# Performance work log

Measured on AMD Instinct MI355X. Metric: run time of the kernel, lower is better.

## Reference

```python
import jax, jax.numpy as jnp
import numpy as np

DIM = 512
DIM_INNER = 512
NUM_HEADS = 16
HEAD_DIM = DIM_INNER // NUM_HEADS  # 32


def setup_inputs() -> dict:
    key = jax.random.key(0)
    k1, k2, k3, k4 = jax.random.split(key, 4)
    b, n = 1, 4096
    x = jax.random.normal(k1, (b, n, DIM), dtype=jnp.float32)
    # torch nn.Linear weights, stored as (in, out) so y = x @ W (+ b)
    s_qkv = 1.0 / np.sqrt(DIM)
    W_qkv = jax.random.uniform(k2, (DIM, DIM_INNER * 3), jnp.float32, -s_qkv, s_qkv)
    W_a = jax.random.uniform(k3, (DIM, NUM_HEADS * 2), jnp.float32, -s_qkv, s_qkv)
    b_a = jax.random.uniform(k4, (NUM_HEADS * 2,), jnp.float32, -s_qkv, s_qkv)
    return {"x": x, "W_qkv": W_qkv, "W_a": W_a, "b_a": b_a}


def _gate_loop(q, k, v, a):
    # q,k,v: (bh, n, d) float32; a: (bh, n, 1, 1) complex64
    kv = jnp.einsum('bnd,bne->bnde', k, v).astype(jnp.complex64)  # (bh, n, d, d)

    def binop(ei, ej):
        a_i, kv_i = ei
        a_j, kv_j = ej
        return a_j * a_i, a_j * kv_i + kv_j

    _, kv = jax.lax.associative_scan(binop, (a, kv), axis=1)
    return jnp.einsum('bnd,bnde->bne', q, kv.real)


def reference(x, W_qkv, W_a, b_a):
    b, n, _ = x.shape
    h, d = NUM_HEADS, HEAD_DIM

    qkv = x @ W_qkv                                   # (b, n, 3*dim_inner)
    q, k, v = jnp.split(qkv, 3, axis=-1)

    def to_heads(t):  # 'b n (h d) -> (b h) n d'
        return t.reshape(b, n, h, d).transpose(0, 2, 1, 3).reshape(b * h, n, d)

    q, k, v = map(to_heads, (q, k, v))

    a_lin = x @ W_a + b_a                             # (b, n, 2h)
    a_ri = a_lin.reshape(b, n, h, 2)
    a_c = jax.lax.complex(a_ri[..., 0], a_ri[..., 1])  # (b, n, h)
    mag = jnp.abs(a_c)
    ph = jnp.angle(a_c)
    gate = jax.lax.complex(jnp.cos(ph), jnp.sin(ph)) * jax.nn.sigmoid(mag).astype(jnp.complex64)
    gate = gate.transpose(0, 2, 1).reshape(b * h, n, 1, 1)  # '(b h) n 1 1'

    out = _gate_loop(q, k, v, gate)                   # (bh, n, d)
    out = out.reshape(b, h, n, d).transpose(0, 2, 1, 3).reshape(b, n, h * d)
    # out_proj is Identity since dim_inner == dim
    return out
```

## Files before the change

kernel.cpp:

```cpp
#include <hip/hip_runtime.h>
#include <hip/hip_bf16.h>

#define SEQ    4096
#define DIM    512
#define DIM3   1536
#define NH     16
#define HD     32
#define CHUNK  64
#define NCHUNK (SEQ / CHUNK)

typedef __attribute__((ext_vector_type(8))) short short8;
typedef __attribute__((ext_vector_type(4))) float f32x4;
typedef __attribute__((ext_vector_type(4))) unsigned short u16x4;
typedef __attribute__((ext_vector_type(4))) unsigned int u32x4;

__device__ inline unsigned short f2bf(float f) {
  unsigned u = __builtin_bit_cast(unsigned, f);
  unsigned r = (u + 0x7fff + ((u >> 16) & 1)) >> 16;
  return (unsigned short)r;
}
__device__ inline float bf2f(unsigned short b) {
  unsigned u = ((unsigned)b) << 16;
  return __builtin_bit_cast(float, u);
}

__global__ __launch_bounds__(256) void gl_cvt_gate(
    const float* __restrict__ x, const float* __restrict__ W,
    const float* __restrict__ Wa, const float* __restrict__ ba,
    unsigned short* __restrict__ xb, unsigned short* __restrict__ Wt,
    float2* __restrict__ graw) {
  __shared__ union {
    float wtile[32][33];
    struct { float xs[4][DIM]; float red[4][8][32]; } g;
  } sm;
  int b = blockIdx.x;
  if (b < 1024) {
    const int n0 = b * 4;
    const int tid = threadIdx.x;
    const float4* xv = (const float4*)(x + (size_t)n0 * DIM);
    u16x4* xbo = (u16x4*)(xb + (size_t)n0 * DIM);
    float4* xsv = (float4*)&sm.g.xs[0][0];
    for (int i = tid; i < 512; i += 256) {
      float4 v = xv[i];
      xsv[i] = v;
      u16x4 o = {f2bf(v.x), f2bf(v.y), f2bf(v.z), f2bf(v.w)};
      xbo[i] = o;
    }
    __syncthreads();
    const int o = tid & 31, s = tid >> 5;
    float pr[4] = {0, 0, 0, 0};
    for (int k = s * 64; k < s * 64 + 64; ++k) {
      float w = Wa[k * 32 + o];
      #pragma unroll
      for (int r = 0; r < 4; ++r) pr[r] += sm.g.xs[r][k] * w;
    }
    #pragma unroll
    for (int r = 0; r < 4; ++r) sm.g.red[r][s][o] = pr[r];
    __syncthreads();
    if (tid < 128) {
      int r = tid >> 5, oo = tid & 31;
      float acc = ba[oo];
      #pragma unroll
      for (int ss = 0; ss < 8; ++ss) acc += sm.g.red[r][ss][oo];
      sm.g.red[r][0][oo] = acc;
    }
    __syncthreads();
    if (tid < 64) {
      int r = tid >> 4, hh = tid & 15;
      float re = sm.g.red[r][0][2 * hh], im = sm.g.red[r][0][2 * hh + 1];
      float mag = sqrtf(re * re + im * im);
      float lml = -log1pf(expf(-mag));
      float ph = atan2f(im, re);
      graw[(size_t)hh * SEQ + n0 + r] = make_float2(lml, ph);
    }
  } else {
    b -= 1024;
    int bx = b % 48, by = b / 48;
    int tx = threadIdx.x & 31, ty = threadIdx.x >> 5;
    for (int i = ty; i < 32; i += 8)
      sm.wtile[i][tx] = W[(size_t)(by * 32 + i) * DIM3 + bx * 32 + tx];
    __syncthreads();
    for (int i = ty; i < 32; i += 8)
      Wt[(size_t)(bx * 32 + i) * DIM + by * 32 + tx] = f2bf(sm.wtile[tx][i]);
  }
}

#define GBM 64
#define GBN 128
#define GBK 64
__global__ __launch_bounds__(256) void gl_gemm_mfma(
    const unsigned short* __restrict__ A, const unsigned short* __restrict__ Bt,
    unsigned short* __restrict__ C) {
  __shared__ unsigned short As[2][GBM * GBK];
  __shared__ unsigned short Bs[2][GBN * GBK];
  const int tid = threadIdx.x;
  const int id = blockIdx.x;
  const int tile = (id & 7) * 96 + (id >> 3);
  const int by = tile / 12, bx = tile % 12;
  const int row0 = by * GBM, col0 = bx * GBN;
  const int wid = tid >> 6, lane = tid & 63;
  const int wr = wid >> 1, wc = wid & 1;
  const int lr = lane & 15, lg = lane >> 4;

  auto stage = [&](int buf, int t) {
    const int k0 = t * GBK;
    #pragma unroll
    for (int i = 0; i < 2; ++i) {
      int byteoff = i * 4096 + tid * 16;
      int row = byteoff >> 7;
      int logslot = ((byteoff >> 4) & 7) ^ (row & 7);
      const unsigned short* gp = A + (size_t)(row0 + row) * DIM + k0 + logslot * 8;
      __builtin_amdgcn_global_load_lds(
          (const __attribute__((address_space(1))) void*)gp,
          (__attribute__((address_space(3))) void*)((char*)As[buf] + byteoff),
          16, 0, 0);
    }
    #pragma unroll
    for (int i = 0; i < 4; ++i) {
      int byteoff = i * 4096 + tid * 16;
      int row = byteoff >> 7;
      int logslot = ((byteoff >> 4) & 7) ^ (row & 7);
      const unsigned short* gp = Bt + (size_t)(col0 + row) * DIM + k0 + logslot * 8;
      __builtin_amdgcn_global_load_lds(
          (const __attribute__((address_space(1))) void*)gp,
          (__attribute__((address_space(3))) void*)((char*)Bs[buf] + byteoff),
          16, 0, 0);
    }
  };

  f32x4 acc[2][4] = {};
  stage(0, 0);

  #pragma unroll
  for (int t = 0; t < 8; ++t) {
    const int p = t & 1;
    if (t < 7) {
      stage(p ^ 1, t + 1);
      asm volatile("s_waitcnt vmcnt(6)" ::: "memory");
    } else {
      asm volatile("s_waitcnt vmcnt(0)" ::: "memory");
    }
    __syncthreads();
    const char* AsB = (const char*)As[p];
    const char* BsB = (const char*)Bs[p];
    #pragma unroll
    for (int ks = 0; ks < 2; ++ks) {
      short8 af[2], bfr[4];
      #pragma unroll
      for (int m = 0; m < 2; ++m) {
        int row = wr * 32 + m * 16 + lr;
        int ps = (ks * 4 + lg) ^ (row & 7);
        af[m] = *(const short8*)(AsB + row * 128 + ps * 16);
      }
      #pragma unroll
      for (int n = 0; n < 4; ++n) {
        int col = wc * 64 + n * 16 + lr;
        int ps = (ks * 4 + lg) ^ (col & 7);
        bfr[n] = *(const short8*)(BsB + col * 128 + ps * 16);
      }
      #pragma unroll
      for (int m = 0; m < 2; ++m)
        #pragma unroll
        for (int n = 0; n < 4; ++n)
          acc[m][n] = __builtin_amdgcn_mfma_f32_16x16x32_bf16(
              af[m], bfr[n], acc[m][n], 0, 0, 0);
    }
    __syncthreads();
  }

  #pragma unroll
  for (int m = 0; m < 2; ++m)
    #pragma unroll
    for (int n = 0; n < 4; ++n) {
      int grow0 = row0 + wr * 32 + m * 16 + lg * 4;
      int gcol = col0 + wc * 64 + n * 16 + lr;
      #pragma unroll
      for (int j = 0; j < 4; ++j)
        C[(size_t)(grow0 + j) * DIM3 + gcol] = f2bf(acc[m][n][j]);
    }
}

__global__ __launch_bounds__(128) void gl_pass1(
    const unsigned short* __restrict__ qkv, const float2* __restrict__ graw,
    float2* __restrict__ LmPh, float* __restrict__ SLre,
    float* __restrict__ SLim, float2* __restrict__ Aprod) {
  const int b = blockIdx.x;
  const int c = b & (NCHUNK - 1), h = b >> 6;
  const int tid = threadIdx.x, w = tid >> 6, lane = tid & 63;
  const int lr = lane & 15, lg = lane >> 4;
  const int n0 = c * CHUNK;
  __shared__ float2 lmph[CHUNK];

  float2 g = graw[(size_t)h * SEQ + n0 + lane];
  float lm = g.x, ph = g.y;
  #pragma unroll
  for (int off = 1; off < 64; off <<= 1) {
    float a = __shfl_up(lm, off), p = __shfl_up(ph, off);
    if (lane >= off) { lm += a; ph += p; }
  }
  if (w == 0) {
    LmPh[(size_t)h * SEQ + n0 + lane] = make_float2(lm, ph);
    lmph[lane] = make_float2(lm, ph);
    if (lane == 63) {
      float e = __expf(lm);
      Aprod[h * NCHUNK + c] = make_float2(e * __cosf(ph), e * __sinf(ph));
    }
  }
  __syncthreads();
  const float2 end = lmph[63];

  const size_t rowb = (size_t)n0 * DIM3 + h * HD;
  f32x4 acc[2][2] = {};
  #pragma unroll
  for (int ks = 0; ks < 2; ++ks) {
    const int jb = ks * 32 + lg * 8;
    float wv[8];
    #pragma unroll
    for (int jj = 0; jj < 8; ++jj) {
      float2 lp = lmph[jb + jj];
      float e = __expf(end.x - lp.x);
      float an = end.y - lp.y;
      wv[jj] = e * (w == 0 ? __cosf(an) : __sinf(an));
    }
    short8 afr[2], bfr[2];
    #pragma unroll
    for (int mt = 0; mt < 2; ++mt) {
      int d = mt * 16 + lr;
      unsigned u0, u1, u2, u3;
      #define LD_KW(q) ((unsigned)f2bf(bf2f(qkv[rowb + (size_t)(jb + 2*(q)) * DIM3 + DIM + d]) * wv[2*(q)]) | \
                        ((unsigned)f2bf(bf2f(qkv[rowb + (size_t)(jb + 2*(q)+1) * DIM3 + DIM + d]) * wv[2*(q)+1]) << 16))
      u0 = LD_KW(0); u1 = LD_KW(1); u2 = LD_KW(2); u3 = LD_KW(3);
      #undef LD_KW
      u32x4 t = {u0, u1, u2, u3};
      afr[mt] = __builtin_bit_cast(short8, t);
    }
    #pragma unroll
    for (int nt = 0; nt < 2; ++nt) {
      int e_ = nt * 16 + lr;
      unsigned u0, u1, u2, u3;
      #define LD_V(q) ((unsigned)qkv[rowb + (size_t)(jb + 2*(q)) * DIM3 + 2*DIM + e_] | \
                       ((unsigned)qkv[rowb + (size_t)(jb + 2*(q)+1) * DIM3 + 2*DIM + e_] << 16))
      u0 = LD_V(0); u1 = LD_V(1); u2 = LD_V(2); u3 = LD_V(3);
      #undef LD_V
      u32x4 t = {u0, u1, u2, u3};
      bfr[nt] = __builtin_bit_cast(short8, t);
    }
    #pragma unroll
    for (int mt = 0; mt < 2; ++mt)
      #pragma unroll
      for (int nt = 0; nt < 2; ++nt)
        acc[mt][nt] = __builtin_amdgcn_mfma_f32_16x16x32_bf16(
            afr[mt], bfr[nt], acc[mt][nt], 0, 0, 0);
  }
  float* dst = (w == 0) ? SLre : SLim;
  const size_t base = (size_t)(h * NCHUNK + c) * (HD * HD);
  #pragma unroll
  for (int mt = 0; mt < 2; ++mt)
    #pragma unroll
    for (int nt = 0; nt < 2; ++nt)
      #pragma unroll
      for (int r = 0; r < 4; ++r) {
        int d = mt * 16 + lg * 4 + r, e_ = nt * 16 + lr;
        dst[base + d * HD + e_] = acc[mt][nt][r];
      }
}

__global__ __launch_bounds__(128) void gl_scan_chunks(
    const float* __restrict__ SLre, const float* __restrict__ SLim,
    const float2* __restrict__ Aprod, unsigned* __restrict__ SinPre,
    unsigned* __restrict__ SinPim) {
  const int h = blockIdx.x >> 3;
  const int oct = blockIdx.x & 7;
  const int tid = threadIdx.x;
  const int elem = oct * 128 + tid;
  const int e = elem & 31;
  const int qp = elem >> 6;
  const bool lo = !(tid & 32);
  const size_t hb = (size_t)h * NCHUNK * (HD * HD) + elem;
  const float2* AP = Aprod + h * NCHUNK;
  float2 s = make_float2(0.f, 0.f);
  for (int cg = 0; cg < NCHUNK; cg += 8) {
    float lre[8], lim[8];
    float2 a[8];
    #pragma unroll
    for (int j = 0; j < 8; ++j) {
      size_t off = hb + (size_t)(cg + j) * (HD * HD);
      lre[j] = SLre[off];
      lim[j] = SLim[off];
      a[j] = AP[cg + j];
    }
    #pragma unroll
    for (int j = 0; j < 8; ++j) {
      float px = __shfl_xor(s.x, 32);
      float py = __shfl_xor(s.y, 32);
      if (lo) {
        size_t wo = (size_t)(h * NCHUNK + cg + j) * 512 + qp * 32 + e;
        SinPre[wo] = (unsigned)f2bf(s.x) | ((unsigned)f2bf(px) << 16);
        SinPim[wo] = (unsigned)f2bf(s.y) | ((unsigned)f2bf(py) << 16);
      }
      float re = s.x, im = s.y;
      s.x = a[j].x * re - a[j].y * im + lre[j];
      s.y = a[j].x * im + a[j].y * re + lim[j];
    }
  }
}

__global__ __launch_bounds__(128) void gl_pass2(
    const unsigned short* __restrict__ qkv, const float2* __restrict__ LmPh,
    const unsigned* __restrict__ SinPre, const unsigned* __restrict__ SinPim,
    float* __restrict__ out) {
  const int b = blockIdx.x;
  const int c = b & (NCHUNK - 1), h = b >> 6;
  const int tid = threadIdx.x, w = tid >> 6, lane = tid & 63;
  const int lr = lane & 15, lg = lane >> 4;
  const int n0 = c * CHUNK;
  __shared__ float2 lmph[CHUNK];
  __shared__ unsigned Pp[32][68];
  if (tid < 64) lmph[tid] = LmPh[(size_t)h * SEQ + n0 + tid];
  __syncthreads();

  const size_t rowb = (size_t)n0 * DIM3 + h * HD;
  short8 kf[2], qf[4];
  #pragma unroll
  for (int mt = 0; mt < 2; ++mt) {
    int j = (2 * w + mt) * 16 + lr;
    kf[mt] = *(const short8*)(qkv + rowb + (size_t)j * DIM3 + DIM + lg * 8);
  }
  #pragma unroll
  for (int nt = 0; nt < 4; ++nt) {
    int n = nt * 16 + lr;
    qf[nt] = *(const short8*)(qkv + rowb + (size_t)n * DIM3 + lg * 8);
  }
  f32x4 pacc[2][4] = {};
  #pragma unroll
  for (int mt = 0; mt < 2; ++mt)
    #pragma unroll
    for (int nt = 0; nt < 4; ++nt)
      pacc[mt][nt] = __builtin_amdgcn_mfma_f32_16x16x32_bf16(
          kf[mt], qf[nt], pacc[mt][nt], 0, 0, 0);

  #pragma unroll
  for (int mt = 0; mt < 2; ++mt) {
    int jt = 2 * w + mt;
    #pragma unroll
    for (int r2 = 0; r2 < 2; ++r2) {
      int j0 = jt * 16 + lg * 4 + 2 * r2;
      float2 lj0 = lmph[j0], lj1 = lmph[j0 + 1];
      #pragma unroll
      for (int nt = 0; nt < 4; ++nt) {
        int n = nt * 16 + lr;
        float2 ln = lmph[n];
        float w0 = (j0 <= n) ? __expf(ln.x - lj0.x) * __cosf(ln.y - lj0.y) : 0.f;
        float w1 = (j0 + 1 <= n) ? __expf(ln.x - lj1.x) * __cosf(ln.y - lj1.y) : 0.f;
        Pp[jt * 8 + lg * 2 + r2][n] =
            (unsigned)f2bf(pacc[mt][nt][2 * r2] * w0) |
            ((unsigned)f2bf(pacc[mt][nt][2 * r2 + 1] * w1) << 16);
      }
    }
  }
  __syncthreads();

  const size_t s512 = (size_t)(h * NCHUNK + c) * 512;
  short8 sre[2], sim[2];
  #pragma unroll
  for (int nt = 0; nt < 2; ++nt) {
    int e_ = nt * 16 + lr;
    unsigned ur[4], ui[4];
    #pragma unroll
    for (int q = 0; q < 4; ++q) {
      ur[q] = SinPre[s512 + (size_t)(lg * 4 + q) * 32 + e_];
      ui[q] = SinPim[s512 + (size_t)(lg * 4 + q) * 32 + e_];
    }
    u32x4 tr = {ur[0], ur[1], ur[2], ur[3]};
    u32x4 ti = {ui[0], ui[1], ui[2], ui[3]};
    sre[nt] = __builtin_bit_cast(short8, tr);
    sim[nt] = __builtin_bit_cast(short8, ti);
  }
  f32x4 ore[2][2] = {}, oim[2][2] = {};
  #pragma unroll
  for (int mt = 0; mt < 2; ++mt)
    #pragma unroll
    for (int nt = 0; nt < 2; ++nt) {
      ore[mt][nt] = __builtin_amdgcn_mfma_f32_16x16x32_bf16(
          qf[2 * w + mt], sre[nt], ore[mt][nt], 0, 0, 0);
      oim[mt][nt] = __builtin_amdgcn_mfma_f32_16x16x32_bf16(
          qf[2 * w + mt], sim[nt], oim[mt][nt], 0, 0, 0);
    }
  f32x4 oacc[2][2];
  #pragma unroll
  for (int mt = 0; mt < 2; ++mt)
    #pragma unroll
    for (int r = 0; r < 4; ++r) {
      int n = (2 * w + mt) * 16 + lg * 4 + r;
      float2 ln = lmph[n];
      float eg = __expf(ln.x);
      float gr = eg * __cosf(ln.y), gi = eg * __sinf(ln.y);
      oacc[mt][0][r] = gr * ore[mt][0][r] - gi * oim[mt][0][r];
      oacc[mt][1][r] = gr * ore[mt][1][r] - gi * oim[mt][1][r];
    }
  #pragma unroll
  for (int ks = 0; ks < 2; ++ks) {
    short8 pa[2];
    #pragma unroll
    for (int mt = 0; mt < 2; ++mt) {
      int n_ = (2 * w + mt) * 16 + lr;
      unsigned u0 = Pp[ks * 16 + lg * 4 + 0][n_];
      unsigned u1 = Pp[ks * 16 + lg * 4 + 1][n_];
      unsigned u2 = Pp[ks * 16 + lg * 4 + 2][n_];
      unsigned u3 = Pp[ks * 16 + lg * 4 + 3][n_];
      u32x4 t = {u0, u1, u2, u3};
      pa[mt] = __builtin_bit_cast(short8, t);
    }
    const int jb = ks * 32 + lg * 8;
    short8 vf[2];
    #pragma unroll
    for (int nt = 0; nt < 2; ++nt) {
      int e_ = nt * 16 + lr;
      unsigned u0, u1, u2, u3;
      #define LD_V(q) ((unsigned)qkv[rowb + (size_t)(jb + 2*(q)) * DIM3 + 2*DIM + e_] | \
                       ((unsigned)qkv[rowb + (size_t)(jb + 2*(q)+1) * DIM3 + 2*DIM + e_] << 16))
      u0 = LD_V(0); u1 = LD_V(1); u2 = LD_V(2); u3 = LD_V(3);
      #undef LD_V
      u32x4 t = {u0, u1, u2, u3};
      vf[nt] = __builtin_bit_cast(short8, t);
    }
    #pragma unroll
    for (int mt = 0; mt < 2; ++mt)
      #pragma unroll
      for (int nt = 0; nt < 2; ++nt)
        oacc[mt][nt] = __builtin_amdgcn_mfma_f32_16x16x32_bf16(
            pa[mt], vf[nt], oacc[mt][nt], 0, 0, 0);
  }
  #pragma unroll
  for (int mt = 0; mt < 2; ++mt)
    #pragma unroll
    for (int nt = 0; nt < 2; ++nt)
      #pragma unroll
      for (int r = 0; r < 4; ++r) {
        int n = (2 * w + mt) * 16 + lg * 4 + r;
        int e_ = nt * 16 + lr;
        out[(size_t)(n0 + n) * DIM + h * HD + e_] = oacc[mt][nt][r];
      }
}

extern "C" void kernel_launch(void* const* d_in, const int* in_sizes, int n_in,
                              void* d_out, int out_size, void* d_ws,
                              size_t ws_size, hipStream_t stream) {
  const float* x     = (const float*)d_in[0];
  const float* W_qkv = (const float*)d_in[1];
  const float* W_a   = (const float*)d_in[2];
  const float* b_a   = (const float*)d_in[3];
  float* out = (float*)d_out;

  char* ws = (char*)d_ws;
  unsigned short* qkv  = (unsigned short*)ws;
  float2* graw  = (float2*)(ws + 12582912);
  float2* LmPh  = (float2*)(ws + 13107200);
  float*  SLre  = (float*)(ws + 13631488);
  float*  SLim  = (float*)(ws + 17825792);
  float2* Aprod = (float2*)(ws + 22020096);
  unsigned* SinPre = (unsigned*)(ws + 22028288);
  unsigned* SinPim = (unsigned*)(ws + 24125440);
  unsigned short* xb = (unsigned short*)(ws + 26222592);
  unsigned short* Wt = (unsigned short*)(ws + 30416896);

  gl_cvt_gate<<<1792, 256, 0, stream>>>(x, W_qkv, W_a, b_a, xb, Wt, graw);
  gl_gemm_mfma<<<768, 256, 0, stream>>>(xb, Wt, qkv);
  gl_pass1<<<NCHUNK * NH, 128, 0, stream>>>(qkv, graw, LmPh, SLre, SLim, Aprod);
  gl_scan_chunks<<<128, 128, 0, stream>>>(SLre, SLim, Aprod, SinPre, SinPim);
  gl_pass2<<<NCHUNK * NH, 128, 0, stream>>>(qkv, LmPh, SinPre, SinPim, out);
}
```

Measured before the change: 52.84 us.

## Fuse chunk passes into cooperative kernel with grid syncs; enlarge GEMM tile

Replaces the three chunked-scan kernels (pass1, chunk scan, pass2) with one cooperative kernel. Each block handles two chunks of a head, keeps K/V and the gate prefix sums in shared memory across phases, and separates the phases with grid-wide syncs. This removes two kernel launches and the reload of K/V and gate data between passes. The QKV GEMM tile also grows from 64x128 to 128x128, halving the block count and giving each wave more MFMA work. The risks are the cost of grid.sync, only 128 of 512 blocks working during the scan phase, and higher register pressure in the GEMM.

```diff
diff --git a/kernel.cpp b/kernel.cpp
--- a/kernel.cpp
+++ b/kernel.cpp
@@ -1,5 +1,8 @@
 #include <hip/hip_runtime.h>
 #include <hip/hip_bf16.h>
+#include <hip/hip_cooperative_groups.h>
+
+namespace cg = cooperative_groups;
 
 #define SEQ    4096
 #define DIM    512
@@ -85,17 +88,17 @@
   }
 }
 
-#define GBM 64
+#define GBM 128
 #define GBN 128
 #define GBK 64
 __global__ __launch_bounds__(256) void gl_gemm_mfma(
     const unsigned short* __restrict__ A, const unsigned short* __restrict__ Bt,
     unsigned short* __restrict__ C) {
   __shared__ unsigned short As[2][GBM * GBK];
-  __shared__ unsigned short Bs[2][GBN * GBK];
+  __shared__ unsigned short Bs[2][GBM * GBK];
   const int tid = threadIdx.x;
   const int id = blockIdx.x;
-  const int tile = (id & 7) * 96 + (id >> 3);
+  const int tile = (id & 7) * 48 + (id >> 3);
   const int by = tile / 12, bx = tile % 12;
   const int row0 = by * GBM, col0 = bx * GBN;
   const int wid = tid >> 6, lane = tid & 63;
@@ -105,7 +108,7 @@
   auto stage = [&](int buf, int t) {
     const int k0 = t * GBK;
     #pragma unroll
-    for (int i = 0; i < 2; ++i) {
+    for (int i = 0; i < 4; ++i) {
       int byteoff = i * 4096 + tid * 16;
       int row = byteoff >> 7;
       int logslot = ((byteoff >> 4) & 7) ^ (row & 7);
@@ -128,7 +131,7 @@
     }
   };
 
-  f32x4 acc[2][4] = {};
+  f32x4 acc[4][4] = {};
   stage(0, 0);
 
   #pragma unroll
@@ -136,7 +139,7 @@
     const int p = t & 1;
     if (t < 7) {
       stage(p ^ 1, t + 1);
-      asm volatile("s_waitcnt vmcnt(6)" ::: "memory");
+      asm volatile("s_waitcnt vmcnt(8)" ::: "memory");
     } else {
       asm volatile("s_waitcnt vmcnt(0)" ::: "memory");
     }
@@ -145,10 +148,10 @@
     const char* BsB = (const char*)Bs[p];
     #pragma unroll
     for (int ks = 0; ks < 2; ++ks) {
-      short8 af[2], bfr[4];
-      #pragma unroll
-      for (int m = 0; m < 2; ++m) {
-        int row = wr * 32 + m * 16 + lr;
+      short8 af[4], bfr[4];
+      #pragma unroll
+      for (int m = 0; m < 4; ++m) {
+        int row = wr * 64 + m * 16 + lr;
         int ps = (ks * 4 + lg) ^ (row & 7);
         af[m] = *(const short8*)(AsB + row * 128 + ps * 16);
       }
@@ -159,7 +162,7 @@
         bfr[n] = *(const short8*)(BsB + col * 128 + ps * 16);
       }
       #pragma unroll
-      for (int m = 0; m < 2; ++m)
+      for (int m = 0; m < 4; ++m)
         #pragma unroll
         for (int n = 0; n < 4; ++n)
           acc[m][n] = __builtin_amdgcn_mfma_f32_16x16x32_bf16(
@@ -169,15 +172,287 @@
   }
 
   #pragma unroll
-  for (int m = 0; m < 2; ++m)
+  for (int m = 0; m < 4; ++m)
     #pragma unroll
     for (int n = 0; n < 4; ++n) {
-      int grow0 = row0 + wr * 32 + m * 16 + lg * 4;
+      int grow0 = row0 + wr * 64 + m * 16 + lg * 4;
       int gcol = col0 + wc * 64 + n * 16 + lr;
       #pragma unroll
       for (int j = 0; j < 4; ++j)
         C[(size_t)(grow0 + j) * DIM3 + gcol] = f2bf(acc[m][n][j]);
     }
+}
+
+__global__ __launch_bounds__(128) void gl_fused(
+    const unsigned short* __restrict__ qkv, const float2* __restrict__ graw,
+    float* __restrict__ SLre, float* __restrict__ SLim,
+    float2* __restrict__ Aprod, unsigned* __restrict__ SinPre,
+    unsigned* __restrict__ SinPim, float* __restrict__ out) {
+  cg::grid_group grid = cg::this_grid();
+  const int b = blockIdx.x;
+  const int tid = threadIdx.x, w = tid >> 6, lane = tid & 63;
+  const int lr = lane & 15, lg = lane >> 4;
+  const int h = b >> 5;
+  const int c0 = (b & 31) * 2;
+
+  __shared__ unsigned short Ksm[2][CHUNK][HD];
+  __shared__ unsigned short Vsm[2][CHUNK][HD];
+  __shared__ float2 lmph[2][CHUNK];
+  __shared__ unsigned Pp[32][68];
+
+  {
+    const int c = c0 + w;
+    float2 g = graw[(size_t)h * SEQ + c * CHUNK + lane];
+    float lm = g.x, ph = g.y;
+    #pragma unroll
+    for (int off = 1; off < 64; off <<= 1) {
+      float a = __shfl_up(lm, off), p = __shfl_up(ph, off);
+      if (lane >= off) { lm += a; ph += p; }
+    }
+    lmph[w][lane] = make_float2(lm, ph);
+    if (lane == 63) {
+      float e = __expf(lm);
+      Aprod[h * NCHUNK + c] = make_float2(e * __cosf(ph), e * __sinf(ph));
+    }
+  }
+
+  #pragma unroll
+  for (int cc = 0; cc < 2; ++cc) {
+    const size_t rb = (size_t)(c0 + cc) * CHUNK * DIM3 + h * HD;
+    for (int i = tid; i < CHUNK * HD / 4; i += 128) {
+      int row = i >> 3, e4 = (i & 7) * 4;
+      *(u16x4*)&Ksm[cc][row][e4] =
+          *(const u16x4*)(qkv + rb + (size_t)row * DIM3 + DIM + e4);
+      *(u16x4*)&Vsm[cc][row][e4] =
+          *(const u16x4*)(qkv + rb + (size_t)row * DIM3 + 2 * DIM + e4);
+    }
+  }
+  __syncthreads();
+
+  #pragma unroll
+  for (int cc = 0; cc < 2; ++cc) {
+    const float2 end = lmph[cc][63];
+    f32x4 acc[2][2] = {};
+    #pragma unroll
+    for (int ks = 0; ks < 2; ++ks) {
+      const int jb = ks * 32 + lg * 8;
+      float wv[8];
+      #pragma unroll
+      for (int jj = 0; jj < 8; ++jj) {
+        float2 lp = lmph[cc][jb + jj];
+        float e = __expf(end.x - lp.x);
+        float an = end.y - lp.y;
+        wv[jj] = e * (w == 0 ? __cosf(an) : __sinf(an));
+      }
+      short8 afr[2], bfr[2];
+      #pragma unroll
+      for (int mt = 0; mt < 2; ++mt) {
+        int d = mt * 16 + lr;
+        unsigned uu[4];
+        #pragma unroll
+        for (int q = 0; q < 4; ++q)
+          uu[q] = (unsigned)f2bf(bf2f(Ksm[cc][jb + 2 * q][d]) * wv[2 * q]) |
+                  ((unsigned)f2bf(bf2f(Ksm[cc][jb + 2 * q + 1][d]) * wv[2 * q + 1]) << 16);
+        u32x4 t = {uu[0], uu[1], uu[2], uu[3]};
+        afr[mt] = __builtin_bit_cast(short8, t);
+      }
+      #pragma unroll
+      for (int nt = 0; nt < 2; ++nt) {
+        int e_ = nt * 16 + lr;
+        unsigned uu[4];
+        #pragma unroll
+        for (int q = 0; q < 4; ++q)
+          uu[q] = (unsigned)Vsm[cc][jb + 2 * q][e_] |
+                  ((unsigned)Vsm[cc][jb + 2 * q + 1][e_] << 16);
+        u32x4 t = {uu[0], uu[1], uu[2], uu[3]};
+        bfr[nt] = __builtin_bit_cast(short8, t);
+      }
+      #pragma unroll
+      for (int mt = 0; mt < 2; ++mt)
+        #pragma unroll
+        for (int nt = 0; nt < 2; ++nt)
+          acc[mt][nt] = __builtin_amdgcn_mfma_f32_16x16x32_bf16(
+              afr[mt], bfr[nt], acc[mt][nt], 0, 0, 0);
+    }
+    float* dst = (w == 0) ? SLre : SLim;
+    const size_t base = (size_t)(h * NCHUNK + c0 + cc) * (HD * HD);
+    #pragma unroll
+    for (int mt = 0; mt < 2; ++mt)
+      #pragma unroll
+      for (int nt = 0; nt < 2; ++nt)
+        #pragma unroll
+        for (int r = 0; r < 4; ++r) {
+          int d = mt * 16 + lg * 4 + r, e_ = nt * 16 + lr;
+          dst[base + d * HD + e_] = acc[mt][nt][r];
+        }
+  }
+  grid.sync();
+
+  if (b < 128) {
+    const int sh = b >> 3;
+    const int oct = b & 7;
+    const int elem = oct * 128 + tid;
+    const int e = elem & 31;
+    const int qp = elem >> 6;
+    const bool lo = !(tid & 32);
+    const size_t hb = (size_t)sh * NCHUNK * (HD * HD) + elem;
+    const float2* AP = Aprod + sh * NCHUNK;
+    float2 s = make_float2(0.f, 0.f);
+    for (int cgp = 0; cgp < NCHUNK; cgp += 8) {
+      float lre[8], lim[8];
+      float2 a[8];
+      #pragma unroll
+      for (int j = 0; j < 8; ++j) {
+        size_t off = hb + (size_t)(cgp + j) * (HD * HD);
+        lre[j] = SLre[off];
+        lim[j] = SLim[off];
+        a[j] = AP[cgp + j];
+      }
+      #pragma unroll
+      for (int j = 0; j < 8; ++j) {
+        float px = __shfl_xor(s.x, 32);
+        float py = __shfl_xor(s.y, 32);
+        if (lo) {
+          size_t wo = (size_t)(sh * NCHUNK + cgp + j) * 512 + qp * 32 + e;
+          SinPre[wo] = (unsigned)f2bf(s.x) | ((unsigned)f2bf(px) << 16);
+          SinPim[wo] = (unsigned)f2bf(s.y) | ((unsigned)f2bf(py) << 16);
+        }
+        float re = s.x, im = s.y;
+        s.x = a[j].x * re - a[j].y * im + lre[j];
+        s.y = a[j].x * im + a[j].y * re + lim[j];
+      }
+    }
+  }
+  grid.sync();
+
+  #pragma unroll
+  for (int cc = 0; cc < 2; ++cc) {
+    const int c = c0 + cc;
+    const int n0 = c * CHUNK;
+    const size_t rowb = (size_t)n0 * DIM3 + h * HD;
+    short8 kf[2], qf[4];
+    #pragma unroll
+    for (int mt = 0; mt < 2; ++mt) {
+      int j = (2 * w + mt) * 16 + lr;
+      kf[mt] = *(const short8*)&Ksm[cc][j][lg * 8];
+    }
+    #pragma unroll
+    for (int nt = 0; nt < 4; ++nt) {
+      int n = nt * 16 + lr;
+      qf[nt] = *(const short8*)(qkv + rowb + (size_t)n * DIM3 + lg * 8);
+    }
+    f32x4 pacc[2][4] = {};
+    #pragma unroll
+    for (int mt = 0; mt < 2; ++mt)
+      #pragma unroll
+      for (int nt = 0; nt < 4; ++nt)
+        pacc[mt][nt] = __builtin_amdgcn_mfma_f32_16x16x32_bf16(
+            kf[mt], qf[nt], pacc[mt][nt], 0, 0, 0);
+
+    __syncthreads();
+    #pragma unroll
+    for (int mt = 0; mt < 2; ++mt) {
+      int jt = 2 * w + mt;
+      #pragma unroll
+      for (int r2 = 0; r2 < 2; ++r2) {
+        int j0 = jt * 16 + lg * 4 + 2 * r2;
+        float2 lj0 = lmph[cc][j0], lj1 = lmph[cc][j0 + 1];
+        #pragma unroll
+        for (int nt = 0; nt < 4; ++nt) {
+          int n = nt * 16 + lr;
+          float2 ln = lmph[cc][n];
+          float w0 = (j0 <= n) ? __expf(ln.x - lj0.x) * __cosf(ln.y - lj0.y) : 0.f;
+          float w1 = (j0 + 1 <= n) ? __expf(ln.x - lj1.x) * __cosf(ln.y - lj1.y) : 0.f;
+          Pp[jt * 8 + lg * 2 + r2][n] =
+              (unsigned)f2bf(pacc[mt][nt][2 * r2] * w0) |
+              ((unsigned)f2bf(pacc[mt][nt][2 * r2 + 1] * w1) << 16);
+        }
+      }
+    }
+    __syncthreads();
+
+    const size_t s512 = (size_t)(h * NCHUNK + c) * 512;
+    short8 sre[2], sim[2];
+    #pragma unroll
+    for (int nt = 0; nt < 2; ++nt) {
+      int e_ = nt * 16 + lr;
+      unsigned ur[4], ui[4];
+      #pragma unroll
+      for (int q = 0; q < 4; ++q) {
+        ur[q] = SinPre[s512 + (size_t)(lg * 4 + q) * 32 + e_];
+        ui[q] = SinPim[s512 + (size_t)(lg * 4 + q) * 32 + e_];
+      }
+      u32x4 tr = {ur[0], ur[1], ur[2], ur[3]};
+      u32x4 ti = {ui[0], ui[1], ui[2], ui[3]};
+      sre[nt] = __builtin_bit_cast(short8, tr);
+      sim[nt] = __builtin_bit_cast(short8, ti);
+    }
+    f32x4 ore[2][2] = {}, oim[2][2] = {};
+    #pragma unroll
+    for (int mt = 0; mt < 2; ++mt)
+      #pragma unroll
+      for (int nt = 0; nt < 2; ++nt) {
+        ore[mt][nt] = __builtin_amdgcn_mfma_f32_16x16x32_bf16(
+            qf[2 * w + mt], sre[nt], ore[mt][nt], 0, 0, 0);
+        oim[mt][nt] = __builtin_amdgcn_mfma_f32_16x16x32_bf16(
+            qf[2 * w + mt], sim[nt], oim[mt][nt], 0, 0, 0);
+      }
+    f32x4 oacc[2][2];
+    #pragma unroll
+    for (int mt = 0; mt < 2; ++mt)
+      #pragma unroll
+      for (int r = 0; r < 4; ++r) {
+        int n = (2 * w + mt) * 16 + lg * 4 + r;
+        float2 ln = lmph[cc][n];
+        float eg = __expf(ln.x);
+        float gr = eg * __cosf(ln.y), gi = eg * __sinf(ln.y);
+        oacc[mt][0][r] = gr * ore[mt][0][r] - gi * oim[mt][0][r];
+        oacc[mt][1][r] = gr * ore[mt][1][r] - gi * oim[mt][1][r];
+      }
+    #pragma unroll
+    for (int ks = 0; ks < 2; ++ks) {
+      short8 pa[2];
+      #pragma unroll
+      for (int mt = 0; mt < 2; ++mt) {
+        int n_ = (2 * w + mt) * 16 + lr;
+        unsigned u0 = Pp[ks * 16 + lg * 4 + 0][n_];
+        unsigned u1 = Pp[ks * 16 + lg * 4 + 1][n_];
+        unsigned u2 = Pp[ks * 16 + lg * 4 + 2][n_];
+        unsigned u3 = Pp[ks * 16 + lg * 4 + 3][n_];
+        u32x4 t = {u0, u1, u2, u3};
+        pa[mt] = __builtin_bit_cast(short8, t);
+      }
+      const int jb = ks * 32 + lg * 8;
+      short8 vf[2];
+      #pragma unroll
+      for (int nt = 0; nt < 2; ++nt) {
+        int e_ = nt * 16 + lr;
+        unsigned uu[4];
+        #pragma unroll
+        for (int q = 0; q < 4; ++q)
+          uu[q] = (unsigned)Vsm[cc][jb + 2 * q][e_] |
+                  ((unsigned)Vsm[cc][jb + 2 * q + 1][e_] << 16);
+        u32x4 t = {uu[0], uu[1], uu[2], uu[3]};
+        vf[nt] = __builtin_bit_cast(short8, t);
+      }
+      #pragma unroll
+      for (int mt = 0; mt < 2; ++mt)
+        #pragma unroll
+        for (int nt = 0; nt < 2; ++nt)
+          oacc[mt][nt] = __builtin_amdgcn_mfma_f32_16x16x32_bf16(
+              pa[mt], vf[nt], oacc[mt][nt], 0, 0, 0);
+    }
+    #pragma unroll
+    for (int mt = 0; mt < 2; ++mt)
+      #pragma unroll
+      for (int nt = 0; nt < 2; ++nt)
+        #pragma unroll
+        for (int r = 0; r < 4; ++r) {
+          int n = (2 * w + mt) * 16 + lg * 4 + r;
+          int e_ = nt * 16 + lr;
+          out[(size_t)(n0 + n) * DIM + h * HD + e_] = oacc[mt][nt][r];
+        }
+  }
 }
 
 __global__ __launch_bounds__(128) void gl_pass1(
@@ -465,8 +740,15 @@
   unsigned short* Wt = (unsigned short*)(ws + 30416896);
 
   gl_cvt_gate<<<1792, 256, 0, stream>>>(x, W_qkv, W_a, b_a, xb, Wt, graw);
-  gl_gemm_mfma<<<768, 256, 0, stream>>>(xb, Wt, qkv);
-  gl_pass1<<<NCHUNK * NH, 128, 0, stream>>>(qkv, graw, LmPh, SLre, SLim, Aprod);
-  gl_scan_chunks<<<128, 128, 0, stream>>>(SLre, SLim, Aprod, SinPre, SinPim);
-  gl_pass2<<<NCHUNK * NH, 128, 0, stream>>>(qkv, LmPh, SinPre, SinPim, out);
-}
+  gl_gemm_mfma<<<384, 256, 0, stream>>>(xb, Wt, qkv);
+
+  void* kargs[] = {(void*)&qkv, (void*)&graw, (void*)&SLre, (void*)&SLim,
+                   (void*)&Aprod, (void*)&SinPre, (void*)&SinPim, (void*)&out};
+  hipError_t err = hipLaunchCooperativeKernel((void*)gl_fused, dim3(512),
+                                              dim3(128), kargs, 0, stream);
+  if (err != hipSuccess) {
+    gl_pass1<<<NCHUNK * NH, 128, 0, stream>>>(qkv, graw, LmPh, SLre, SLim, Aprod);
+    gl_scan_chunks<<<128, 128, 0, stream>>>(SLre, SLim, Aprod, SinPre, SinPim);
+    gl_pass2<<<NCHUNK * NH, 128, 0, stream>>>(qkv, LmPh, SinPre, SinPim, out);
+  }
+}
```

New measurement: 180.1 us. 3.41x slower.

## Enlarge GEMM M-tile to 128 and stage K/V chunks in LDS for scan passes

Applied to the files above, without the earlier changes.

The QKV GEMM tile grows from 64x128 to 128x128, halving the grid to 384 blocks and doubling per-wave accumulators so operand data is reused more. In pass1 and pass2, K and V chunk slices are now loaded cooperatively into shared memory with vectorized loads, replacing the scattered per-element global 16-bit gathers. The prefix scan in pass1 now runs only in wave 0. The goal is fewer global transactions and better GEMM data reuse, at the cost of fewer GEMM blocks (384 on a 256-CU part, which may leave the second wave partly idle) and more LDS per block.

```diff
diff --git a/kernel.cpp b/kernel.cpp
--- a/kernel.cpp
+++ b/kernel.cpp
@@ -85,17 +85,17 @@
   }
 }
 
-#define GBM 64
+#define GBM 128
 #define GBN 128
 #define GBK 64
 __global__ __launch_bounds__(256) void gl_gemm_mfma(
     const unsigned short* __restrict__ A, const unsigned short* __restrict__ Bt,
     unsigned short* __restrict__ C) {
   __shared__ unsigned short As[2][GBM * GBK];
-  __shared__ unsigned short Bs[2][GBN * GBK];
+  __shared__ unsigned short Bs[2][GBM * GBK];
   const int tid = threadIdx.x;
   const int id = blockIdx.x;
-  const int tile = (id & 7) * 96 + (id >> 3);
+  const int tile = (id & 7) * 48 + (id >> 3);
   const int by = tile / 12, bx = tile % 12;
   const int row0 = by * GBM, col0 = bx * GBN;
   const int wid = tid >> 6, lane = tid & 63;
@@ -105,7 +105,7 @@
   auto stage = [&](int buf, int t) {
     const int k0 = t * GBK;
     #pragma unroll
-    for (int i = 0; i < 2; ++i) {
+    for (int i = 0; i < 4; ++i) {
       int byteoff = i * 4096 + tid * 16;
       int row = byteoff >> 7;
       int logslot = ((byteoff >> 4) & 7) ^ (row & 7);
@@ -128,7 +128,7 @@
     }
   };
 
-  f32x4 acc[2][4] = {};
+  f32x4 acc[4][4] = {};
   stage(0, 0);
 
   #pragma unroll
@@ -136,7 +136,7 @@
     const int p = t & 1;
     if (t < 7) {
       stage(p ^ 1, t + 1);
-      asm volatile("s_waitcnt vmcnt(6)" ::: "memory");
+      asm volatile("s_waitcnt vmcnt(8)" ::: "memory");
     } else {
       asm volatile("s_waitcnt vmcnt(0)" ::: "memory");
     }
@@ -145,10 +145,10 @@
     const char* BsB = (const char*)Bs[p];
     #pragma unroll
     for (int ks = 0; ks < 2; ++ks) {
-      short8 af[2], bfr[4];
-      #pragma unroll
-      for (int m = 0; m < 2; ++m) {
-        int row = wr * 32 + m * 16 + lr;
+      short8 af[4], bfr[4];
+      #pragma unroll
+      for (int m = 0; m < 4; ++m) {
+        int row = wr * 64 + m * 16 + lr;
         int ps = (ks * 4 + lg) ^ (row & 7);
         af[m] = *(const short8*)(AsB + row * 128 + ps * 16);
       }
@@ -159,7 +159,7 @@
         bfr[n] = *(const short8*)(BsB + col * 128 + ps * 16);
       }
       #pragma unroll
-      for (int m = 0; m < 2; ++m)
+      for (int m = 0; m < 4; ++m)
         #pragma unroll
         for (int n = 0; n < 4; ++n)
           acc[m][n] = __builtin_amdgcn_mfma_f32_16x16x32_bf16(
@@ -169,10 +169,10 @@
   }
 
   #pragma unroll
-  for (int m = 0; m < 2; ++m)
+  for (int m = 0; m < 4; ++m)
     #pragma unroll
     for (int n = 0; n < 4; ++n) {
-      int grow0 = row0 + wr * 32 + m * 16 + lg * 4;
+      int grow0 = row0 + wr * 64 + m * 16 + lg * 4;
       int gcol = col0 + wc * 64 + n * 16 + lr;
       #pragma unroll
       for (int j = 0; j < 4; ++j)
@@ -190,17 +190,28 @@
   const int lr = lane & 15, lg = lane >> 4;
   const int n0 = c * CHUNK;
   __shared__ float2 lmph[CHUNK];
-
-  float2 g = graw[(size_t)h * SEQ + n0 + lane];
-  float lm = g.x, ph = g.y;
-  #pragma unroll
-  for (int off = 1; off < 64; off <<= 1) {
-    float a = __shfl_up(lm, off), p = __shfl_up(ph, off);
-    if (lane >= off) { lm += a; ph += p; }
-  }
+  __shared__ unsigned short Ksm[CHUNK][34];
+  __shared__ unsigned short Vsm[CHUNK][34];
+
+  const size_t rb = (size_t)n0 * DIM3 + h * HD;
+  for (int i = tid; i < 512; i += 128) {
+    int row = i >> 3, e4 = (i & 7) * 4;
+    *(u16x4*)&Ksm[row][e4] =
+        *(const u16x4*)(qkv + rb + (size_t)row * DIM3 + DIM + e4);
+    *(u16x4*)&Vsm[row][e4] =
+        *(const u16x4*)(qkv + rb + (size_t)row * DIM3 + 2 * DIM + e4);
+  }
+
   if (w == 0) {
+    float2 g = graw[(size_t)h * SEQ + n0 + lane];
+    float lm = g.x, ph = g.y;
+    #pragma unroll
+    for (int off = 1; off < 64; off <<= 1) {
+      float a = __shfl_up(lm, off), p = __shfl_up(ph, off);
+      if (lane >= off) { lm += a; ph += p; }
+    }
+    lmph[lane] = make_float2(lm, ph);
     LmPh[(size_t)h * SEQ + n0 + lane] = make_float2(lm, ph);
-    lmph[lane] = make_float2(lm, ph);
     if (lane == 63) {
       float e = __expf(lm);
       Aprod[h * NCHUNK + c] = make_float2(e * __cosf(ph), e * __sinf(ph));
@@ -209,7 +220,6 @@
   __syncthreads();
   const float2 end = lmph[63];
 
-  const size_t rowb = (size_t)n0 * DIM3 + h * HD;
   f32x4 acc[2][2] = {};
   #pragma unroll
   for (int ks = 0; ks < 2; ++ks) {
@@ -226,23 +236,23 @@
     #pragma unroll
     for (int mt = 0; mt < 2; ++mt) {
       int d = mt * 16 + lr;
-      unsigned u0, u1, u2, u3;
-      #define LD_KW(q) ((unsigned)f2bf(bf2f(qkv[rowb + (size_t)(jb + 2*(q)) * DIM3 + DIM + d]) * wv[2*(q)]) | \
-                        ((unsigned)f2bf(bf2f(qkv[rowb + (size_t)(jb + 2*(q)+1) * DIM3 + DIM + d]) * wv[2*(q)+1]) << 16))
-      u0 = LD_KW(0); u1 = LD_KW(1); u2 = LD_KW(2); u3 = LD_KW(3);
-      #undef LD_KW
-      u32x4 t = {u0, u1, u2, u3};
+      unsigned uu[4];
+      #pragma unroll
+      for (int q = 0; q < 4; ++q)
+        uu[q] = (unsigned)f2bf(bf2f(Ksm[jb + 2 * q][d]) * wv[2 * q]) |
+                ((unsigned)f2bf(bf2f(Ksm[jb + 2 * q + 1][d]) * wv[2 * q + 1]) << 16);
+      u32x4 t = {uu[0], uu[1], uu[2], uu[3]};
       afr[mt] = __builtin_bit_cast(short8, t);
     }
     #pragma unroll
     for (int nt = 0; nt < 2; ++nt) {
       int e_ = nt * 16 + lr;
-      unsigned u0, u1, u2, u3;
-      #define LD_V(q) ((unsigned)qkv[rowb + (size_t)(jb + 2*(q)) * DIM3 + 2*DIM + e_] | \
-                       ((unsigned)qkv[rowb + (size_t)(jb + 2*(q)+1) * DIM3 + 2*DIM + e_] << 16))
-      u0 = LD_V(0); u1 = LD_V(1); u2 = LD_V(2); u3 = LD_V(3);
-      #undef LD_V
-      u32x4 t = {u0, u1, u2, u3};
+      unsigned uu[4];
+      #pragma unroll
+      for (int q = 0; q < 4; ++q)
+        uu[q] = (unsigned)Vsm[jb + 2 * q][e_] |
+                ((unsigned)Vsm[jb + 2 * q + 1][e_] << 16);
+      u32x4 t = {uu[0], uu[1], uu[2], uu[3]};
       bfr[nt] = __builtin_bit_cast(short8, t);
     }
     #pragma unroll
@@ -316,10 +326,17 @@
   const int n0 = c * CHUNK;
   __shared__ float2 lmph[CHUNK];
   __shared__ unsigned Pp[32][68];
+  __shared__ unsigned short Vsm[CHUNK][34];
+
+  const size_t rowb = (size_t)n0 * DIM3 + h * HD;
+  for (int i = tid; i < 512; i += 128) {
+    int row = i >> 3, e4 = (i & 7) * 4;
+    *(u16x4*)&Vsm[row][e4] =
+        *(const u16x4*)(qkv + rowb + (size_t)row * DIM3 + 2 * DIM + e4);
+  }
   if (tid < 64) lmph[tid] = LmPh[(size_t)h * SEQ + n0 + tid];
   __syncthreads();
 
-  const size_t rowb = (size_t)n0 * DIM3 + h * HD;
   short8 kf[2], qf[4];
   #pragma unroll
   for (int mt = 0; mt < 2; ++mt) {
@@ -416,12 +433,12 @@
     #pragma unroll
     for (int nt = 0; nt < 2; ++nt) {
       int e_ = nt * 16 + lr;
-      unsigned u0, u1, u2, u3;
-      #define LD_V(q) ((unsigned)qkv[rowb + (size_t)(jb + 2*(q)) * DIM3 + 2*DIM + e_] | \
-                       ((unsigned)qkv[rowb + (size_t)(jb + 2*(q)+1) * DIM3 + 2*DIM + e_] << 16))
-      u0 = LD_V(0); u1 = LD_V(1); u2 = LD_V(2); u3 = LD_V(3);
-      #undef LD_V
-      u32x4 t = {u0, u1, u2, u3};
+      unsigned uu[4];
+      #pragma unroll
+      for (int q = 0; q < 4; ++q)
+        uu[q] = (unsigned)Vsm[jb + 2 * q][e_] |
+                ((unsigned)Vsm[jb + 2 * q + 1][e_] << 16);
+      u32x4 t = {uu[0], uu[1], uu[2], uu[3]};
       vf[nt] = __builtin_bit_cast(short8, t);
     }
     #pragma unroll
@@ -465,7 +482,7 @@
   unsigned short* Wt = (unsigned short*)(ws + 30416896);
 
   gl_cvt_gate<<<1792, 256, 0, stream>>>(x, W_qkv, W_a, b_a, xb, Wt, graw);
-  gl_gemm_mfma<<<768, 256, 0, stream>>>(xb, Wt, qkv);
+  gl_gemm_mfma<<<384, 256, 0, stream>>>(xb, Wt, qkv);
   gl_pass1<<<NCHUNK * NH, 128, 0, stream>>>(qkv, graw, LmPh, SLre, SLim, Aprod);
   gl_scan_chunks<<<128, 128, 0, stream>>>(SLre, SLim, Aprod, SinPre, SinPim);
   gl_pass2<<<NCHUNK * NH, 128, 0, stream>>>(qkv, LmPh, SinPre, SinPim, out);
```

New measurement: 54.36 us. 1.03x slower.
